# Kernel tuning notes

Measured on AMD Instinct MI355X. Metric: run time of the kernel, lower is better.

The kernel has to match this reference:

```python
import jax, jax.numpy as jnp
import numpy as np

D_MODEL = 256
N_HEAD = 8
D_FF = 1024
B = 8
N_PER = 4096
NQ = B * N_PER
L = 16
NEG_INF = -1e9
EPS = 1e-5


def layer_norm(x, g, b):
    mu = jnp.mean(x, axis=-1, keepdims=True)
    var = jnp.mean(jnp.square(x - mu), axis=-1, keepdims=True)
    return (x - mu) * jax.lax.rsqrt(var + EPS) * g + b


def setup_inputs() -> dict:
    key = jax.random.key(0)
    ks = jax.random.split(key, 20)
    s = 1.0 / np.sqrt(D_MODEL)
    sf = 1.0 / np.sqrt(D_FF)
    inp = {
        "src": jax.random.normal(ks[0], (NQ, D_MODEL), jnp.float32),
        "pos": jax.random.normal(ks[1], (NQ, D_MODEL), jnp.float32),
        # per-batch-relative neighbor indices in [-1, N_PER); -1 == invalid/padded
        "index_pair": jax.random.randint(ks[2], (NQ, L), 0, N_PER + 1, jnp.int32) - 1,
        "query_batch_cnt": jnp.full((B,), N_PER, jnp.int32),
        "key_batch_cnt": jnp.full((B,), N_PER, jnp.int32),
        "index_pair_batch": (jnp.arange(NQ, dtype=jnp.int32) // N_PER).astype(jnp.int32),
        "Wq": jax.random.normal(ks[3], (D_MODEL, D_MODEL), jnp.float32) * s,
        "bq": jnp.zeros((D_MODEL,), jnp.float32),
        "Wk": jax.random.normal(ks[4], (D_MODEL, D_MODEL), jnp.float32) * s,
        "bk": jnp.zeros((D_MODEL,), jnp.float32),
        "Wv": jax.random.normal(ks[5], (D_MODEL, D_MODEL), jnp.float32) * s,
        "bv": jnp.zeros((D_MODEL,), jnp.float32),
        "Wo": jax.random.normal(ks[6], (D_MODEL, D_MODEL), jnp.float32) * s,
        "bo": jnp.zeros((D_MODEL,), jnp.float32),
        "W1": jax.random.normal(ks[7], (D_MODEL, D_FF), jnp.float32) * s,
        "b1": jnp.zeros((D_FF,), jnp.float32),
        "W2": jax.random.normal(ks[8], (D_FF, D_MODEL), jnp.float32) * sf,
        "b2": jnp.zeros((D_MODEL,), jnp.float32),
        "g1": jnp.ones((D_MODEL,), jnp.float32),
        "be1": jnp.zeros((D_MODEL,), jnp.float32),
        "g2": jnp.ones((D_MODEL,), jnp.float32),
        "be2": jnp.zeros((D_MODEL,), jnp.float32),
    }
    return inp


def local_attn(q, k, v, index_pair, key_batch_cnt, index_pair_batch,
               Wq, bq, Wk, bk, Wv, bv, Wo, bo):
    H, hd = N_HEAD, D_MODEL // N_HEAD
    scale = 1.0 / np.sqrt(hd)
    qh = (q @ Wq + bq).reshape(NQ, H, hd) * scale        # [Nq,H,hd]
    kh = (k @ Wk + bk).reshape(NQ, H, hd)                # [Nk,H,hd] (Nk==Nq)
    vh = (v @ Wv + bv).reshape(NQ, H, hd)
    # start offset of each batch's keys in the stacked key tensor
    offs = jnp.cumsum(key_batch_cnt) - key_batch_cnt      # [B]
    valid = index_pair >= 0                               # [Nq,L]
    gidx = jnp.where(valid, index_pair + offs[index_pair_batch][:, None], 0)
    k_g = kh[gidx]                                        # [Nq,L,H,hd]
    v_g = vh[gidx]                                        # [Nq,L,H,hd]
    logits = jnp.einsum('nhd,nlhd->nhl', qh, k_g)         # [Nq,H,L]
    logits = jnp.where(valid[:, None, :], logits, NEG_INF)
    attn = jax.nn.softmax(logits, axis=-1)
    out = jnp.einsum('nhl,nlhd->nhd', attn, v_g).reshape(NQ, D_MODEL)
    return out @ Wo + bo


def reference(src, pos, index_pair, query_batch_cnt, key_batch_cnt, index_pair_batch,
              Wq, bq, Wk, bk, Wv, bv, Wo, bo, W1, b1, W2, b2, g1, be1, g2, be2):
    # forward_post (normalize_before=False), dropout==0 (eval)
    qk = src + pos
    src2 = local_attn(qk, qk, src, index_pair, key_batch_cnt, index_pair_batch,
                      Wq, bq, Wk, bk, Wv, bv, Wo, bo)
    x = layer_norm(src + src2, g1, be1)
    ff = jax.nn.relu(x @ W1 + b1) @ W2 + b2
    return layer_norm(x + ff, g2, be2)
```

## Files before the change

### kernel.cpp

```cpp
#include <hip/hip_runtime.h>
#include <hip/hip_bf16.h>
#include <cstdint>
#include <cstddef>

#define NQ_ 32768
#define DM_ 256
#define DFF_ 1024
#define LNB_ 16
#define NB_ 8

typedef __attribute__((ext_vector_type(4))) float f32x4;
typedef __attribute__((ext_vector_type(8))) short s16x8;

__device__ __forceinline__ float bf2f(ushort u) {
    union { unsigned int i; float f; } c; c.i = ((unsigned int)u) << 16; return c.f;
}
__device__ __forceinline__ ushort f2bf(float f) {
    union { float f; unsigned int i; } c; c.f = f;
    unsigned int x = c.i;
    return (ushort)((x + 0x7fffu + ((x >> 16) & 1u)) >> 16);
}


__global__ __launch_bounds__(256) void prep_all(const float* __restrict__ src, const float* __restrict__ pos,
                                                ushort* __restrict__ qkb, ushort* __restrict__ srcb,
                                                const float* __restrict__ Wq, const float* __restrict__ Wk,
                                                const float* __restrict__ Wv, const float* __restrict__ Wo,
                                                const float* __restrict__ W1, const float* __restrict__ W2,
                                                const int* __restrict__ kbc,
                                                const float* __restrict__ bq, const float* __restrict__ bk,
                                                ushort* __restrict__ WqT, ushort* __restrict__ WkT,
                                                ushort* __restrict__ WvT, ushort* __restrict__ WoT,
                                                ushort* __restrict__ W1T, ushort* __restrict__ W2T,
                                                int* __restrict__ offs, float* __restrict__ bias2) {
    const int blk = blockIdx.x;
    const int t = threadIdx.x;
    if (blk < 8192) {
        const int i = (blk * 256 + t) * 4;
        float4 s = *(const float4*)(src + i);
        float4 p = *(const float4*)(pos + i);
        ushort4 a, b;
        a.x = f2bf(s.x + p.x); a.y = f2bf(s.y + p.y); a.z = f2bf(s.z + p.z); a.w = f2bf(s.w + p.w);
        b.x = f2bf(s.x);       b.y = f2bf(s.y);       b.z = f2bf(s.z);       b.w = f2bf(s.w);
        *(ushort4*)(qkb + i) = a;
        *(ushort4*)(srcb + i) = b;
        return;
    }
    if (blk == 8384) {
        if (t == 0) { int a = 0; for (int i = 0; i < NB_; ++i) { offs[i] = a; a += kbc[i]; } }
        bias2[t] = bq[t];
        bias2[256 + t] = bk[t];
        return;
    }
    __shared__ float tile[64][65];
    const int tb = blk - 8192;
    const float* W; ushort* Wt; int K, N, kt, ntl;
    if (tb < 64) {
        const int sec = tb >> 4;
        W  = sec == 0 ? Wq  : sec == 1 ? Wk  : sec == 2 ? Wv  : Wo;
        Wt = sec == 0 ? WqT : sec == 1 ? WkT : sec == 2 ? WvT : WoT;
        K = 256; N = 256; kt = (tb & 15) >> 2; ntl = tb & 3;
    } else if (tb < 128) {
        W = W1; Wt = W1T; K = 256; N = 1024;
        const int r = tb - 64; kt = r >> 4; ntl = r & 15;
    } else {
        W = W2; Wt = W2T; K = 1024; N = 256;
        const int r = tb - 128; kt = r >> 2; ntl = r & 3;
    }
    const int k0 = kt * 64, n0 = ntl * 64;
    const int r16 = t >> 4, c4 = (t & 15) * 4;
#pragma unroll
    for (int p = 0; p < 4; ++p) {
        const int row = p * 16 + r16;
        float4 v = *(const float4*)(W + (long)(k0 + row) * N + n0 + c4);
        tile[row][c4] = v.x; tile[row][c4 + 1] = v.y; tile[row][c4 + 2] = v.z; tile[row][c4 + 3] = v.w;
    }
    __syncthreads();
#pragma unroll
    for (int p = 0; p < 4; ++p) {
        const int orow = p * 16 + r16;
        ushort4 o;
        o.x = f2bf(tile[c4][orow]);
        o.y = f2bf(tile[c4 + 1][orow]);
        o.z = f2bf(tile[c4 + 2][orow]);
        o.w = f2bf(tile[c4 + 3][orow]);
        *(ushort4*)(Wt + (long)(n0 + orow) * K + k0 + c4) = o;
    }
}


__device__ __forceinline__ void gld_lds16(const ushort* g, ushort* l) {
    __builtin_amdgcn_global_load_lds((const __attribute__((address_space(1))) void*)g,
                                     (__attribute__((address_space(3))) void*)l, 16, 0, 0);
}


template <bool RELU>
__global__ __launch_bounds__(256) void gemm_kernel(const ushort* __restrict__ A, const ushort* __restrict__ Bt,
                                                   const float* __restrict__ bias, ushort* __restrict__ C,
                                                   int M, int N, int K, float alpha) {
    __shared__ __align__(16) ushort As[2 * 2 * 128 * 32];
    __shared__ __align__(16) ushort Bs[2 * 2 * 128 * 32];
    const int tid = threadIdx.x;
    const int lane = tid & 63;
    const int wave = tid >> 6;
    const int wr = wave >> 1, wc = wave & 1;

    const int b = (int)(blockIdx.y * gridDim.x + blockIdx.x);
    const int idx = b >> 3;
    const int xt = (b & 7) * 32 + (idx & 31);
    const int yt = idx >> 5;
    const long m0 = (long)xt * 128;
    const long n0 = (long)yt * 128;

    f32x4 acc[4][4] = {};

    const int rel8 = ((tid & 3) ^ ((tid >> 3) & 3)) * 8;
    const ushort* Ar0 = A + (m0 + (tid >> 2)) * K + rel8;
    const ushort* Ar1 = Ar0 + 64 * K;
    const ushort* Br0 = Bt + (n0 + (tid >> 2)) * K + rel8;
    const ushort* Br1 = Br0 + 64 * K;
    const int la = lane & 15;
    const int sx = ((lane >> 4) ^ ((la >> 1) & 3)) * 8;

    const int nt = K >> 6;
    int buf = 0;
#pragma unroll
    for (int p = 0; p < 2; ++p) {
        gld_lds16(Ar0 + p * 32, As + p * 4096 + tid * 8);
        gld_lds16(Ar1 + p * 32, As + p * 4096 + (tid + 256) * 8);
        gld_lds16(Br0 + p * 32, Bs + p * 4096 + tid * 8);
        gld_lds16(Br1 + p * 32, Bs + p * 4096 + (tid + 256) * 8);
    }

    for (int t = 0; t < nt; ++t) {
        const int bO = buf * 8192;
        if (t + 1 < nt) {
            const int kt = (t + 1) << 6;
            const int nO = (buf ^ 1) * 8192;
#pragma unroll
            for (int p = 0; p < 2; ++p) {
                gld_lds16(Ar0 + kt + p * 32, As + nO + p * 4096 + tid * 8);
                gld_lds16(Ar1 + kt + p * 32, As + nO + p * 4096 + (tid + 256) * 8);
                gld_lds16(Br0 + kt + p * 32, Bs + nO + p * 4096 + tid * 8);
                gld_lds16(Br1 + kt + p * 32, Bs + nO + p * 4096 + (tid + 256) * 8);
            }
            asm volatile("s_waitcnt vmcnt(8)" ::: "memory");
        } else {
            asm volatile("s_waitcnt vmcnt(0)" ::: "memory");
        }
        __builtin_amdgcn_s_barrier();
        s16x8 af[2][4], bfr[2][4];
#pragma unroll
        for (int kk = 0; kk < 2; ++kk) {
#pragma unroll
            for (int m = 0; m < 4; ++m)
                af[kk][m] = *(const s16x8*)(As + bO + kk * 4096 + (wr * 64 + m * 16 + la) * 32 + sx);
#pragma unroll
            for (int n = 0; n < 4; ++n)
                bfr[kk][n] = *(const s16x8*)(Bs + bO + kk * 4096 + (wc * 64 + n * 16 + la) * 32 + sx);
        }
        asm volatile("s_waitcnt lgkmcnt(0)" ::: "memory");
        __builtin_amdgcn_s_barrier();
#pragma unroll
        for (int kk = 0; kk < 2; ++kk)
#pragma unroll
            for (int m = 0; m < 4; ++m)
#pragma unroll
                for (int n = 0; n < 4; ++n)
                    acc[m][n] = __builtin_amdgcn_mfma_f32_16x16x32_bf16(af[kk][m], bfr[kk][n], acc[m][n], 0, 0, 0);
        buf ^= 1;
    }

#pragma unroll
    for (int n = 0; n < 4; ++n) {
        const long col = n0 + wc * 64 + n * 16 + la;
        const float bv = bias[col];
#pragma unroll
        for (int m = 0; m < 4; ++m) {
#pragma unroll
            for (int j = 0; j < 4; ++j) {
                const long row = m0 + wr * 64 + m * 16 + (lane >> 4) * 4 + j;
                float r = (acc[m][n][j] + bv) * alpha;
                if (RELU) r = fmaxf(r, 0.f);
                C[row * N + col] = f2bf(r);
            }
        }
    }
}


__global__ __launch_bounds__(256) void qkv_kernel(const ushort* __restrict__ qkb, const ushort* __restrict__ srcb,
                                                  const ushort* __restrict__ WqkT, const ushort* __restrict__ WvT,
                                                  const float* __restrict__ bias2, const float* __restrict__ bv,
                                                  ushort* __restrict__ QKb, ushort* __restrict__ Vb) {
    __shared__ __align__(16) ushort As[2 * 2 * 128 * 32];
    __shared__ __align__(16) ushort Bs[2 * 2 * 128 * 32];
    const int tid = threadIdx.x;
    const int lane = tid & 63;
    const int wave = tid >> 6;
    const int wr = wave >> 1, wc = wave & 1;
    const int K = DM_;

    const bool isqk = blockIdx.y < 4;
    const ushort* A  = isqk ? qkb : srcb;
    const ushort* Bt = isqk ? WqkT : WvT;
    const float* bias = isqk ? bias2 : bv;
    ushort* C = isqk ? QKb : Vb;
    const int N = isqk ? 512 : 256;
    const int bx = (int)blockIdx.x;
    const int xt = (bx & 7) * 32 + (bx >> 3);
    const long m0 = (long)xt * 128;
    const long n0 = (long)(isqk ? blockIdx.y : (blockIdx.y - 4)) * 128;

    f32x4 acc[4][4] = {};

    const int rel8 = ((tid & 3) ^ ((tid >> 3) & 3)) * 8;
    const ushort* Ar0 = A + (m0 + (tid >> 2)) * K + rel8;
    const ushort* Ar1 = Ar0 + 64 * K;
    const ushort* Br0 = Bt + (n0 + (tid >> 2)) * K + rel8;
    const ushort* Br1 = Br0 + 64 * K;
    const int la = lane & 15;
    const int sx = ((lane >> 4) ^ ((la >> 1) & 3)) * 8;

    const int nt = K >> 6;
    int buf = 0;
#pragma unroll
    for (int p = 0; p < 2; ++p) {
        gld_lds16(Ar0 + p * 32, As + p * 4096 + tid * 8);
        gld_lds16(Ar1 + p * 32, As + p * 4096 + (tid + 256) * 8);
        gld_lds16(Br0 + p * 32, Bs + p * 4096 + tid * 8);
        gld_lds16(Br1 + p * 32, Bs + p * 4096 + (tid + 256) * 8);
    }

    for (int t = 0; t < nt; ++t) {
        const int bO = buf * 8192;
        if (t + 1 < nt) {
            const int kt = (t + 1) << 6;
            const int nO = (buf ^ 1) * 8192;
#pragma unroll
            for (int p = 0; p < 2; ++p) {
                gld_lds16(Ar0 + kt + p * 32, As + nO + p * 4096 + tid * 8);
                gld_lds16(Ar1 + kt + p * 32, As + nO + p * 4096 + (tid + 256) * 8);
                gld_lds16(Br0 + kt + p * 32, Bs + nO + p * 4096 + tid * 8);
                gld_lds16(Br1 + kt + p * 32, Bs + nO + p * 4096 + (tid + 256) * 8);
            }
            asm volatile("s_waitcnt vmcnt(8)" ::: "memory");
        } else {
            asm volatile("s_waitcnt vmcnt(0)" ::: "memory");
        }
        __builtin_amdgcn_s_barrier();
        s16x8 af[2][4], bfr[2][4];
#pragma unroll
        for (int kk = 0; kk < 2; ++kk) {
#pragma unroll
            for (int m = 0; m < 4; ++m)
                af[kk][m] = *(const s16x8*)(As + bO + kk * 4096 + (wr * 64 + m * 16 + la) * 32 + sx);
#pragma unroll
            for (int n = 0; n < 4; ++n)
                bfr[kk][n] = *(const s16x8*)(Bs + bO + kk * 4096 + (wc * 64 + n * 16 + la) * 32 + sx);
        }
        asm volatile("s_waitcnt lgkmcnt(0)" ::: "memory");
        __builtin_amdgcn_s_barrier();
#pragma unroll
        for (int kk = 0; kk < 2; ++kk)
#pragma unroll
            for (int m = 0; m < 4; ++m)
#pragma unroll
                for (int n = 0; n < 4; ++n)
                    acc[m][n] = __builtin_amdgcn_mfma_f32_16x16x32_bf16(af[kk][m], bfr[kk][n], acc[m][n], 0, 0, 0);
        buf ^= 1;
    }

#pragma unroll
    for (int n = 0; n < 4; ++n) {
        const long col = n0 + wc * 64 + n * 16 + la;
        const float bvv = bias[col];
#pragma unroll
        for (int m = 0; m < 4; ++m) {
#pragma unroll
            for (int j = 0; j < 4; ++j) {
                const long row = m0 + wr * 64 + m * 16 + (lane >> 4) * 4 + j;
                C[row * N + col] = f2bf(acc[m][n][j] + bvv);
            }
        }
    }
}


template <bool F32OUT>
__global__ __launch_bounds__(256) void gemm_ln_kernel(const ushort* __restrict__ A, const ushort* __restrict__ Bt,
                                                      const float* __restrict__ bias,
                                                      const ushort* __restrict__ resid,
                                                      const float* __restrict__ g, const float* __restrict__ be,
                                                      void* __restrict__ outv, int K) {
    __shared__ __align__(16) ushort As[2 * 2 * 64 * 32];
    __shared__ __align__(16) ushort Bs[2 * 2 * 256 * 32];
    const int tid = threadIdx.x;
    const int lane = tid & 63;
    const int wave = tid >> 6;
    const long m0 = (long)blockIdx.x * 64;

    const int rel8 = ((tid & 3) ^ ((tid >> 3) & 3)) * 8;
    const int arow = tid >> 2;
    const ushort* Asrc = A + (m0 + arow) * K + rel8;
    const ushort* Bsrc[4];
#pragma unroll
    for (int j = 0; j < 4; ++j)
        Bsrc[j] = Bt + (long)(arow + 64 * j) * K + rel8;

    const int la = lane & 15;
    const int sx = ((lane >> 4) ^ ((la >> 1) & 3)) * 8;

    f32x4 acc[4][4] = {};
    const int nt = K >> 6;
    int buf = 0;
#pragma unroll
    for (int p = 0; p < 2; ++p)
        gld_lds16(Asrc + p * 32, As + (p * 256 + tid) * 8);
#pragma unroll
    for (int i = 0; i < 8; ++i)
        gld_lds16(Bsrc[i & 3] + (i >> 2) * 32, Bs + ((i >> 2) * 1024 + (i & 3) * 256 + tid) * 8);

    for (int t = 0; t < nt; ++t) {
        const int bA = buf * 4096, bB = buf * 16384;
        if (t + 1 < nt) {
            const int kt = (t + 1) << 6;
            const int nA = (buf ^ 1) * 4096, nB = (buf ^ 1) * 16384;
#pragma unroll
            for (int p = 0; p < 2; ++p)
                gld_lds16(Asrc + kt + p * 32, As + nA + (p * 256 + tid) * 8);
#pragma unroll
            for (int i = 0; i < 8; ++i)
                gld_lds16(Bsrc[i & 3] + kt + (i >> 2) * 32, Bs + nB + ((i >> 2) * 1024 + (i & 3) * 256 + tid) * 8);
            asm volatile("s_waitcnt vmcnt(10)" ::: "memory");
        } else {
            asm volatile("s_waitcnt vmcnt(0)" ::: "memory");
        }
        __builtin_amdgcn_s_barrier();
        s16x8 af[2][4], bfr[2][4];
#pragma unroll
        for (int kk = 0; kk < 2; ++kk) {
#pragma unroll
            for (int m = 0; m < 4; ++m)
                af[kk][m] = *(const s16x8*)(As + bA + kk * 2048 + (m * 16 + la) * 32 + sx);
#pragma unroll
            for (int n = 0; n < 4; ++n)
                bfr[kk][n] = *(const s16x8*)(Bs + bB + kk * 8192 + (wave * 64 + n * 16 + la) * 32 + sx);
        }
        asm volatile("s_waitcnt lgkmcnt(0)" ::: "memory");
        __builtin_amdgcn_s_barrier();
#pragma unroll
        for (int kk = 0; kk < 2; ++kk)
#pragma unroll
            for (int m = 0; m < 4; ++m)
#pragma unroll
                for (int n = 0; n < 4; ++n)
                    acc[m][n] = __builtin_amdgcn_mfma_f32_16x16x32_bf16(af[kk][m], bfr[kk][n], acc[m][n], 0, 0, 0);
        buf ^= 1;
    }

    float* red_s = (float*)As;
    float* red_q = (float*)As + 256;
    const int rg4 = (lane >> 4) * 4;
    float bv[4];
#pragma unroll
    for (int n = 0; n < 4; ++n) bv[n] = bias[wave * 64 + n * 16 + la];

#pragma unroll
    for (int m = 0; m < 4; ++m) {
#pragma unroll
        for (int j = 0; j < 4; ++j) {
            const int lr = m * 16 + rg4 + j;
            float s = 0.f, q = 0.f;
#pragma unroll
            for (int n = 0; n < 4; ++n) {
                const int col = wave * 64 + n * 16 + la;
                float v = acc[m][n][j] + bv[n] + bf2f(resid[(m0 + lr) * DM_ + col]);
                acc[m][n][j] = v;
                s += v; q += v * v;
            }
#pragma unroll
            for (int mk = 1; mk < 16; mk <<= 1) { s += __shfl_xor(s, mk); q += __shfl_xor(q, mk); }
            if (la == 0) { red_s[wave * 64 + lr] = s; red_q[wave * 64 + lr] = q; }
        }
    }
    __syncthreads();

    float gv[4], bev[4];
#pragma unroll
    for (int n = 0; n < 4; ++n) {
        const int col = wave * 64 + n * 16 + la;
        gv[n] = g[col]; bev[n] = be[col];
    }
#pragma unroll
    for (int m = 0; m < 4; ++m) {
#pragma unroll
        for (int j = 0; j < 4; ++j) {
            const int lr = m * 16 + rg4 + j;
            const float s = red_s[lr] + red_s[64 + lr] + red_s[128 + lr] + red_s[192 + lr];
            const float q = red_q[lr] + red_q[64 + lr] + red_q[128 + lr] + red_q[192 + lr];
            const float mu = s * (1.f / 256.f);
            const float rsig = rsqrtf(q * (1.f / 256.f) - mu * mu + 1e-5f);
#pragma unroll
            for (int n = 0; n < 4; ++n) {
                const int col = wave * 64 + n * 16 + la;
                const float r = (acc[m][n][j] - mu) * rsig * gv[n] + bev[n];
                if (F32OUT) ((float*)outv)[(m0 + lr) * DM_ + col] = r;
                else        ((ushort*)outv)[(m0 + lr) * DM_ + col] = f2bf(r);
            }
        }
    }
}


__global__ __launch_bounds__(256, 4) void attn_kernel(const ushort* __restrict__ QKb,
                                                      const ushort* __restrict__ Vb, const int* __restrict__ ipair,
                                                      const int* __restrict__ ipb, const int* __restrict__ offs,
                                                      ushort* __restrict__ Ob) {
    const int blk = (blockIdx.x & 7) * (NQ_ / 8 / 8) + (blockIdx.x >> 3);
    const int lane = threadIdx.x & 63;
    const int n = blk * 8 + (threadIdx.x >> 6) * 2 + (lane >> 5);
    const size_t hoff = (size_t)(lane & 31) * 8;

    int ip[LNB_];
#pragma unroll
    for (int c = 0; c < 4; ++c) {
        int4 v = *(const int4*)(ipair + n * LNB_ + c * 4);
        ip[c * 4] = v.x; ip[c * 4 + 1] = v.y; ip[c * 4 + 2] = v.z; ip[c * 4 + 3] = v.w;
    }
    float q[8];
    {
        s16x8 v = *(const s16x8*)(QKb + (size_t)n * 512 + hoff);
#pragma unroll
        for (int e = 0; e < 8; ++e) q[e] = bf2f((ushort)v[e]);
    }
    const int off = offs[ipb[n]];
    float lg[LNB_];
    s16x8 va[LNB_];
#pragma unroll
    for (int j = 0; j < LNB_; ++j) {
        const int g = ip[j] >= 0 ? ip[j] + off : 0;
        s16x8 v = *(const s16x8*)(QKb + (size_t)g * 512 + 256 + hoff);
        va[j] = *(const s16x8*)(Vb + (size_t)g * DM_ + hoff);
        float p = 0.f;
#pragma unroll
        for (int e = 0; e < 8; ++e)
            p = fmaf(q[e], bf2f((ushort)v[e]), p);
        p += __shfl_xor(p, 1);
        p += __shfl_xor(p, 2);
        lg[j] = ip[j] >= 0 ? p * 0.17677669529663688f : -1e9f;
    }
    float mx = lg[0];
#pragma unroll
    for (int j = 1; j < LNB_; ++j) mx = fmaxf(mx, lg[j]);
    float sum = 0.f, pw[LNB_];
#pragma unroll
    for (int j = 0; j < LNB_; ++j) { pw[j] = __expf(lg[j] - mx); sum += pw[j]; }
    const float inv = 1.f / sum;

    float acc[8] = {};
#pragma unroll
    for (int j = 0; j < LNB_; ++j) {
        const float w = pw[j] * inv;
#pragma unroll
        for (int e = 0; e < 8; ++e)
            acc[e] = fmaf(w, bf2f((ushort)va[j][e]), acc[e]);
    }
    s16x8 o;
#pragma unroll
    for (int e = 0; e < 8; ++e) o[e] = (short)f2bf(acc[e]);
    *(s16x8*)(Ob + (size_t)n * DM_ + hoff) = o;
}


extern "C" void kernel_launch(void* const* d_in, const int* in_sizes, int n_in,
                              void* d_out, int out_size, void* d_ws, size_t ws_size,
                              hipStream_t stream) {
    const float* src = (const float*)d_in[0];
    const float* pos = (const float*)d_in[1];
    const int* ipair = (const int*)d_in[2];
    const int* kbc   = (const int*)d_in[4];
    const int* ipb   = (const int*)d_in[5];
    const float* Wq = (const float*)d_in[6];  const float* bq = (const float*)d_in[7];
    const float* Wk = (const float*)d_in[8];  const float* bk = (const float*)d_in[9];
    const float* Wv = (const float*)d_in[10]; const float* bv = (const float*)d_in[11];
    const float* Wo = (const float*)d_in[12]; const float* bo = (const float*)d_in[13];
    const float* W1 = (const float*)d_in[14]; const float* b1 = (const float*)d_in[15];
    const float* W2 = (const float*)d_in[16]; const float* b2 = (const float*)d_in[17];
    const float* g1 = (const float*)d_in[18]; const float* be1 = (const float*)d_in[19];
    const float* g2 = (const float*)d_in[20]; const float* be2 = (const float*)d_in[21];

    char* ws = (char*)d_ws;
    const size_t SB = (size_t)NQ_ * DM_ * 2;
    ushort* qkb  = (ushort*)(ws);
    ushort* srcb = (ushort*)(ws + SB);
    ushort* QKb  = (ushort*)(ws + 2 * SB);
    ushort* Vb   = (ushort*)(ws + 4 * SB);
    ushort* hb   = (ushort*)(ws);
    ushort* attno = qkb;
    ushort* xb    = Vb;
    char* wb = ws + 6 * SB;
    ushort* WqT = (ushort*)(wb);
    ushort* WkT = (ushort*)(wb + 131072);
    ushort* WvT = (ushort*)(wb + 262144);
    ushort* WoT = (ushort*)(wb + 393216);
    ushort* W1T = (ushort*)(wb + 524288);
    ushort* W2T = (ushort*)(wb + 1048576);
    int* offs   = (int*)(wb + 1572864);
    float* bias2 = (float*)(wb + 1572864 + 64);

    prep_all<<<8192 + 192 + 1, 256, 0, stream>>>(src, pos, qkb, srcb,
                                                 Wq, Wk, Wv, Wo, W1, W2, kbc, bq, bk,
                                                 WqT, WkT, WvT, WoT, W1T, W2T, offs, bias2);

    dim3 gqkv(256, 6);
    dim3 gff1(NQ_ / 128, DFF_ / 128);
    qkv_kernel<<<gqkv, 256, 0, stream>>>(qkb, srcb, WqT, WvT, bias2, bv, QKb, Vb);
    attn_kernel<<<NQ_ / 8, 256, 0, stream>>>(QKb, Vb, ipair, ipb, offs, attno);
    gemm_ln_kernel<false><<<NQ_ / 64, 256, 0, stream>>>(attno, WoT, bo, srcb, g1, be1, (void*)xb, DM_);
    gemm_kernel<true><<<gff1, 256, 0, stream>>>(xb, W1T, b1, hb, NQ_, DFF_, DM_, 1.f);
    gemm_ln_kernel<true><<<NQ_ / 64, 256, 0, stream>>>(hb, W2T, b2, xb, g2, be2, d_out, DFF_);
}
```

Measured before the change: 162.3 us.

## Enlarge GEMM+LayerNorm tile to 128 rows with 8 waves in 2x4 grid

The fused GEMM+LayerNorm kernel now processes 128 rows per block with 512 threads arranged as 2 row-waves by 4 column-waves, instead of 64 rows with 4 waves. Each weight tile loaded into LDS is reused by twice as many rows, halving B-matrix global traffic per output row, and the load/wait counts and the cross-wave LN reduction are adjusted to match. The cost is a larger LDS footprint and fewer blocks (256 instead of 512), which may reduce occupancy and latency hiding on the many CUs.

```diff
diff --git a/kernel.cpp b/kernel.cpp
--- a/kernel.cpp
+++ b/kernel.cpp
@@ -289,25 +289,25 @@
 
 
 template <bool F32OUT>
-__global__ __launch_bounds__(256) void gemm_ln_kernel(const ushort* __restrict__ A, const ushort* __restrict__ Bt,
-                                                      const float* __restrict__ bias,
-                                                      const ushort* __restrict__ resid,
-                                                      const float* __restrict__ g, const float* __restrict__ be,
-                                                      void* __restrict__ outv, int K) {
-    __shared__ __align__(16) ushort As[2 * 2 * 64 * 32];
+__global__ __launch_bounds__(512, 2) void gemm_ln_kernel(const ushort* __restrict__ A, const ushort* __restrict__ Bt,
+                                                         const float* __restrict__ bias,
+                                                         const ushort* __restrict__ resid,
+                                                         const float* __restrict__ g, const float* __restrict__ be,
+                                                         void* __restrict__ outv, int K) {
+    __shared__ __align__(16) ushort As[2 * 2 * 128 * 32];
     __shared__ __align__(16) ushort Bs[2 * 2 * 256 * 32];
     const int tid = threadIdx.x;
     const int lane = tid & 63;
     const int wave = tid >> 6;
-    const long m0 = (long)blockIdx.x * 64;
+    const int wr = wave >> 2;
+    const int wc = wave & 3;
+    const long m0 = (long)blockIdx.x * 128;
 
     const int rel8 = ((tid & 3) ^ ((tid >> 3) & 3)) * 8;
     const int arow = tid >> 2;
-    const ushort* Asrc = A + (m0 + arow) * K + rel8;
-    const ushort* Bsrc[4];
-#pragma unroll
-    for (int j = 0; j < 4; ++j)
-        Bsrc[j] = Bt + (long)(arow + 64 * j) * K + rel8;
+    const ushort* Asrc  = A + (m0 + arow) * K + rel8;
+    const ushort* Bsrc0 = Bt + (long)arow * K + rel8;
+    const ushort* Bsrc1 = Bt + (long)(arow + 128) * K + rel8;
 
     const int la = lane & 15;
     const int sx = ((lane >> 4) ^ ((la >> 1) & 3)) * 8;
@@ -316,24 +316,24 @@
     const int nt = K >> 6;
     int buf = 0;
 #pragma unroll
-    for (int p = 0; p < 2; ++p)
-        gld_lds16(Asrc + p * 32, As + (p * 256 + tid) * 8);
-#pragma unroll
-    for (int i = 0; i < 8; ++i)
-        gld_lds16(Bsrc[i & 3] + (i >> 2) * 32, Bs + ((i >> 2) * 1024 + (i & 3) * 256 + tid) * 8);
+    for (int p = 0; p < 2; ++p) {
+        gld_lds16(Asrc + p * 32, As + p * 4096 + tid * 8);
+        gld_lds16(Bsrc0 + p * 32, Bs + p * 8192 + tid * 8);
+        gld_lds16(Bsrc1 + p * 32, Bs + p * 8192 + (tid + 512) * 8);
+    }
 
     for (int t = 0; t < nt; ++t) {
-        const int bA = buf * 4096, bB = buf * 16384;
+        const int bA = buf * 8192, bB = buf * 16384;
         if (t + 1 < nt) {
             const int kt = (t + 1) << 6;
-            const int nA = (buf ^ 1) * 4096, nB = (buf ^ 1) * 16384;
-#pragma unroll
-            for (int p = 0; p < 2; ++p)
-                gld_lds16(Asrc + kt + p * 32, As + nA + (p * 256 + tid) * 8);
-#pragma unroll
-            for (int i = 0; i < 8; ++i)
-                gld_lds16(Bsrc[i & 3] + kt + (i >> 2) * 32, Bs + nB + ((i >> 2) * 1024 + (i & 3) * 256 + tid) * 8);
-            asm volatile("s_waitcnt vmcnt(10)" ::: "memory");
+            const int nA = (buf ^ 1) * 8192, nB = (buf ^ 1) * 16384;
+#pragma unroll
+            for (int p = 0; p < 2; ++p) {
+                gld_lds16(Asrc + kt + p * 32, As + nA + p * 4096 + tid * 8);
+                gld_lds16(Bsrc0 + kt + p * 32, Bs + nB + p * 8192 + tid * 8);
+                gld_lds16(Bsrc1 + kt + p * 32, Bs + nB + p * 8192 + (tid + 512) * 8);
+            }
+            asm volatile("s_waitcnt vmcnt(6)" ::: "memory");
         } else {
             asm volatile("s_waitcnt vmcnt(0)" ::: "memory");
         }
@@ -343,10 +343,10 @@
         for (int kk = 0; kk < 2; ++kk) {
 #pragma unroll
             for (int m = 0; m < 4; ++m)
-                af[kk][m] = *(const s16x8*)(As + bA + kk * 2048 + (m * 16 + la) * 32 + sx);
+                af[kk][m] = *(const s16x8*)(As + bA + kk * 4096 + (wr * 64 + m * 16 + la) * 32 + sx);
 #pragma unroll
             for (int n = 0; n < 4; ++n)
-                bfr[kk][n] = *(const s16x8*)(Bs + bB + kk * 8192 + (wave * 64 + n * 16 + la) * 32 + sx);
+                bfr[kk][n] = *(const s16x8*)(Bs + bB + kk * 8192 + (wc * 64 + n * 16 + la) * 32 + sx);
         }
         asm volatile("s_waitcnt lgkmcnt(0)" ::: "memory");
         __builtin_amdgcn_s_barrier();
@@ -361,28 +361,28 @@
     }
 
     float* red_s = (float*)As;
-    float* red_q = (float*)As + 256;
+    float* red_q = (float*)As + 512;
     const int rg4 = (lane >> 4) * 4;
     float bv[4];
 #pragma unroll
-    for (int n = 0; n < 4; ++n) bv[n] = bias[wave * 64 + n * 16 + la];
+    for (int n = 0; n < 4; ++n) bv[n] = bias[wc * 64 + n * 16 + la];
 
 #pragma unroll
     for (int m = 0; m < 4; ++m) {
 #pragma unroll
         for (int j = 0; j < 4; ++j) {
-            const int lr = m * 16 + rg4 + j;
+            const int grow = wr * 64 + m * 16 + rg4 + j;
             float s = 0.f, q = 0.f;
 #pragma unroll
             for (int n = 0; n < 4; ++n) {
-                const int col = wave * 64 + n * 16 + la;
-                float v = acc[m][n][j] + bv[n] + bf2f(resid[(m0 + lr) * DM_ + col]);
+                const int col = wc * 64 + n * 16 + la;
+                float v = acc[m][n][j] + bv[n] + bf2f(resid[(m0 + grow) * DM_ + col]);
                 acc[m][n][j] = v;
                 s += v; q += v * v;
             }
 #pragma unroll
             for (int mk = 1; mk < 16; mk <<= 1) { s += __shfl_xor(s, mk); q += __shfl_xor(q, mk); }
-            if (la == 0) { red_s[wave * 64 + lr] = s; red_q[wave * 64 + lr] = q; }
+            if (la == 0) { red_s[wc * 128 + grow] = s; red_q[wc * 128 + grow] = q; }
         }
     }
     __syncthreads();
@@ -390,24 +390,24 @@
     float gv[4], bev[4];
 #pragma unroll
     for (int n = 0; n < 4; ++n) {
-        const int col = wave * 64 + n * 16 + la;
+        const int col = wc * 64 + n * 16 + la;
         gv[n] = g[col]; bev[n] = be[col];
     }
 #pragma unroll
     for (int m = 0; m < 4; ++m) {
 #pragma unroll
         for (int j = 0; j < 4; ++j) {
-            const int lr = m * 16 + rg4 + j;
-            const float s = red_s[lr] + red_s[64 + lr] + red_s[128 + lr] + red_s[192 + lr];
-            const float q = red_q[lr] + red_q[64 + lr] + red_q[128 + lr] + red_q[192 + lr];
+            const int grow = wr * 64 + m * 16 + rg4 + j;
+            const float s = red_s[grow] + red_s[128 + grow] + red_s[256 + grow] + red_s[384 + grow];
+            const float q = red_q[grow] + red_q[128 + grow] + red_q[256 + grow] + red_q[384 + grow];
             const float mu = s * (1.f / 256.f);
             const float rsig = rsqrtf(q * (1.f / 256.f) - mu * mu + 1e-5f);
 #pragma unroll
             for (int n = 0; n < 4; ++n) {
-                const int col = wave * 64 + n * 16 + la;
+                const int col = wc * 64 + n * 16 + la;
                 const float r = (acc[m][n][j] - mu) * rsig * gv[n] + bev[n];
-                if (F32OUT) ((float*)outv)[(m0 + lr) * DM_ + col] = r;
-                else        ((ushort*)outv)[(m0 + lr) * DM_ + col] = f2bf(r);
+                if (F32OUT) ((float*)outv)[(m0 + grow) * DM_ + col] = r;
+                else        ((ushort*)outv)[(m0 + grow) * DM_ + col] = f2bf(r);
             }
         }
     }
@@ -518,7 +518,7 @@
     dim3 gff1(NQ_ / 128, DFF_ / 128);
     qkv_kernel<<<gqkv, 256, 0, stream>>>(qkb, srcb, WqT, WvT, bias2, bv, QKb, Vb);
     attn_kernel<<<NQ_ / 8, 256, 0, stream>>>(QKb, Vb, ipair, ipb, offs, attno);
-    gemm_ln_kernel<false><<<NQ_ / 64, 256, 0, stream>>>(attno, WoT, bo, srcb, g1, be1, (void*)xb, DM_);
+    gemm_ln_kernel<false><<<NQ_ / 128, 512, 0, stream>>>(attno, WoT, bo, srcb, g1, be1, (void*)xb, DM_);
     gemm_kernel<true><<<gff1, 256, 0, stream>>>(xb, W1T, b1, hb, NQ_, DFF_, DM_, 1.f);
-    gemm_ln_kernel<true><<<NQ_ / 64, 256, 0, stream>>>(hb, W2T, b2, xb, g2, be2, d_out, DFF_);
-}
+    gemm_ln_kernel<true><<<NQ_ / 128, 512, 0, stream>>>(hb, W2T, b2, xb, g2, be2, d_out, DFF_);
+}
```

After: 162.1 us. About the same (-0.1%).
